# Performance work log

Measured on AMD Instinct MI355X. Metric: run time of the kernel, lower is better.

Reference implementation:

```python
import jax, jax.numpy as jnp
import numpy as np

D = 1024        # input_dim
H = 4096        # hidden_dim (expert FFN width)
RH = H // 2     # router hidden
E = 8           # expert_count
TOP_K = 2
N = 4096        # tokens
LN_EPS = 1e-5


def setup_inputs() -> dict:
    key = jax.random.key(0)
    ks = jax.random.split(key, 12)
    s_d = 1.0 / np.sqrt(D)
    s_h = 1.0 / np.sqrt(H)
    s_rh = 1.0 / np.sqrt(RH)
    return {
        "x": jax.random.normal(ks[0], (N, D), jnp.float32),
        "ln_g": jnp.ones((D,), jnp.float32),
        "ln_b": jnp.zeros((D,), jnp.float32),
        # router: Linear(D, RH) -> ReLU -> Linear(RH, E)
        "rw1": jax.random.uniform(ks[1], (D, RH), jnp.float32, -s_d, s_d),
        "rb1": jax.random.uniform(ks[2], (RH,), jnp.float32, -s_d, s_d),
        "rw2": jax.random.uniform(ks[3], (RH, E), jnp.float32, -s_rh, s_rh),
        "rb2": jax.random.uniform(ks[4], (E,), jnp.float32, -s_rh, s_rh),
        # experts: E x (Linear(D, H) -> ReLU -> Linear(H, D)); dropout is identity in eval
        "ew1": jax.random.uniform(ks[5], (E, D, H), jnp.float32, -s_d, s_d),
        "eb1": jax.random.uniform(ks[6], (E, H), jnp.float32, -s_d, s_d),
        "ew2": jax.random.uniform(ks[7], (E, H, D), jnp.float32, -s_h, s_h),
        "eb2": jax.random.uniform(ks[8], (E, D), jnp.float32, -s_h, s_h),
    }


def reference(x, ln_g, ln_b, rw1, rb1, rw2, rb2, ew1, eb1, ew2, eb2):
    residual = x
    # LayerNorm
    mu = jnp.mean(x, axis=-1, keepdims=True)
    var = jnp.mean(jnp.square(x - mu), axis=-1, keepdims=True)
    xn = (x - mu) * jax.lax.rsqrt(var + LN_EPS) * ln_g + ln_b
    # Router MLP + softmax + top-k with renormalized gates
    logits = jax.nn.relu(xn @ rw1 + rb1) @ rw2 + rb2          # [N, E]
    probs = jax.nn.softmax(logits, axis=-1)
    vals, idx = jax.lax.top_k(probs, TOP_K)                    # [N, K]
    vals = vals / jnp.sum(vals, axis=-1, keepdims=True)
    # combine weights per expert: [N, E]
    combine = jnp.sum(jax.nn.one_hot(idx, E, dtype=vals.dtype) * vals[..., None], axis=1)
    # dense grouped expert FFN: h [E, N, H], y [E, N, D]
    h = jax.nn.relu(jnp.einsum("nd,edh->enh", xn, ew1) + eb1[:, None, :])
    y = jnp.einsum("enh,ehd->end", h, ew2) + eb2[:, None, :]
    out = residual + jnp.einsum("end,ne->nd", y, combine)
    return out
```

## Files before the change

kernel.cpp:

```cpp
#include <hip/hip_runtime.h>
#include <stdint.h>

#define D_    1024
#define H_    4096
#define RH_   2048
#define E_    8
#define N_    4096
#define NK_   8192
#define MT256_MAX 39
#define DELTA_MARGIN 1e-4f
#define FIX_CAP 256

typedef __bf16 bf16x8 __attribute__((ext_vector_type(8)));
typedef float  f32x4  __attribute__((ext_vector_type(4)));


__device__ __forceinline__ unsigned short f2bf(float f) {
  union { float f; unsigned u; } v; v.f = f;
  unsigned r = v.u + 0x7fffu + ((v.u >> 16) & 1u);
  return (unsigned short)(r >> 16);
}
__device__ __forceinline__ float bf2f(unsigned short h) {
  union { unsigned u; float f; } v; v.u = ((unsigned)h) << 16;
  return v.f;
}

#define GLOAD16(gp, lp) \
  __builtin_amdgcn_global_load_lds((__attribute__((address_space(1))) void*)(void*)(gp), \
                                   (__attribute__((address_space(3))) void*)(lp), 16, 0, 0)

__global__ __launch_bounds__(256) void k_transpose(const float* __restrict__ in,
                                                   unsigned short* __restrict__ outH,
                                                   unsigned short* __restrict__ outL,
                                                   int R, int C) {
  __shared__ float t[32][33];
  const int b = blockIdx.z;
  const int c0 = blockIdx.x * 32, r0 = blockIdx.y * 32;
  const int lx = threadIdx.x & 31, ly = threadIdx.x >> 5;
  const long inB = (long)R * C;
  #pragma unroll
  for (int i = 0; i < 4; i++) {
    int r = r0 + ly + i * 8;
    t[ly + i * 8][lx] = in[b * inB + (long)r * C + c0 + lx];
  }
  __syncthreads();
  #pragma unroll
  for (int i = 0; i < 4; i++) {
    int c = c0 + ly + i * 8;
    float v = t[lx][ly + i * 8];
    unsigned short h = f2bf(v);
    long oi = b * inB + (long)c * R + r0 + lx;
    outH[oi] = h;
    if (outL) outL[oi] = f2bf(v - bf2f(h));
  }
}

__global__ __launch_bounds__(256) void k_layernorm(const float* __restrict__ x,
                                                   const float* __restrict__ g,
                                                   const float* __restrict__ b,
                                                   unsigned short* __restrict__ xnh,
                                                   unsigned short* __restrict__ xnl) {
  __shared__ float red[4];
  const int n = blockIdx.x, tid = threadIdx.x;
  float4 v = ((const float4*)(x + (long)n * D_))[tid];
  float s = v.x + v.y + v.z + v.w;
  #pragma unroll
  for (int o = 32; o >= 1; o >>= 1) s += __shfl_xor(s, o, 64);
  if ((tid & 63) == 0) red[tid >> 6] = s;
  __syncthreads();
  float mean = (red[0] + red[1] + red[2] + red[3]) * (1.f / D_);
  __syncthreads();
  float d0 = v.x - mean, d1 = v.y - mean, d2 = v.z - mean, d3 = v.w - mean;
  float ss = d0 * d0 + d1 * d1 + d2 * d2 + d3 * d3;
  #pragma unroll
  for (int o = 32; o >= 1; o >>= 1) ss += __shfl_xor(ss, o, 64);
  if ((tid & 63) == 0) red[tid >> 6] = ss;
  __syncthreads();
  float rstd = rsqrtf((red[0] + red[1] + red[2] + red[3]) * (1.f / D_) + 1e-5f);
  float4 gg = ((const float4*)g)[tid];
  float4 bb = ((const float4*)b)[tid];
  float xn0 = d0 * rstd * gg.x + bb.x;
  float xn1 = d1 * rstd * gg.y + bb.y;
  float xn2 = d2 * rstd * gg.z + bb.z;
  float xn3 = d3 * rstd * gg.w + bb.w;
  unsigned short h0 = f2bf(xn0), h1 = f2bf(xn1), h2 = f2bf(xn2), h3 = f2bf(xn3);
  ((ushort4*)xnh)[(long)n * 256 + tid] = make_ushort4(h0, h1, h2, h3);
  ((ushort4*)xnl)[(long)n * 256 + tid] = make_ushort4(
      f2bf(xn0 - bf2f(h0)), f2bf(xn1 - bf2f(h1)),
      f2bf(xn2 - bf2f(h2)), f2bf(xn3 - bf2f(h3)));
}

__global__ void k_init(int* ctl) { if (threadIdx.x < 46) ctl[threadIdx.x] = 0; }

__global__ __launch_bounds__(256) void k_router_gemm(const unsigned short* __restrict__ xh,
                                                     const unsigned short* __restrict__ xl,
                                                     const unsigned short* __restrict__ bhT,
                                                     const unsigned short* __restrict__ blT,
                                                     const float* __restrict__ rb1,
                                                     float* __restrict__ h_r) {
  __shared__ __align__(16) unsigned short Ah[128 * 32], Al[128 * 32], Bh[128 * 32], Bl[128 * 32];
  const int tid = threadIdx.x, lane = tid & 63, wid = tid >> 6;
  const int m0 = blockIdx.x * 128, n0 = blockIdx.y * 128;
  const int wm = wid >> 1, wn = wid & 1;
  const int seg0 = wid * 2;
  const int srow = lane >> 2;
  const int scol = (lane & 3) * 8;
  const long a0 = (long)(m0 + seg0 * 16 + srow) * D_ + scol;
  const long a1 = a0 + 16 * D_;
  const long b0 = (long)(n0 + seg0 * 16 + srow) * D_ + scol;
  const long b1 = b0 + 16 * D_;
  const int rl = lane & 15, kh8 = (lane >> 4) * 8;
  f32x4 acc[4][4];
  #pragma unroll
  for (int i = 0; i < 4; i++)
    #pragma unroll
    for (int j = 0; j < 4; j++) acc[i][j] = 0.f;

  for (int k0 = 0; k0 < D_; k0 += 32) {
    GLOAD16(xh + a0 + k0, Ah + seg0 * 512);
    GLOAD16(xh + a1 + k0, Ah + seg0 * 512 + 512);
    GLOAD16(xl + a0 + k0, Al + seg0 * 512);
    GLOAD16(xl + a1 + k0, Al + seg0 * 512 + 512);
    GLOAD16(bhT + b0 + k0, Bh + seg0 * 512);
    GLOAD16(bhT + b1 + k0, Bh + seg0 * 512 + 512);
    GLOAD16(blT + b0 + k0, Bl + seg0 * 512);
    GLOAD16(blT + b1 + k0, Bl + seg0 * 512 + 512);
    __syncthreads();
    bf16x8 bhf[4], blf[4];
    #pragma unroll
    for (int ni = 0; ni < 4; ni++) {
      int r = (wn * 64 + ni * 16 + rl) * 32 + kh8;
      bhf[ni] = *(const bf16x8*)(Bh + r);
      blf[ni] = *(const bf16x8*)(Bl + r);
    }
    #pragma unroll
    for (int mi = 0; mi < 4; mi++) {
      int r = (wm * 64 + mi * 16 + rl) * 32 + kh8;
      bf16x8 ah = *(const bf16x8*)(Ah + r);
      bf16x8 al = *(const bf16x8*)(Al + r);
      #pragma unroll
      for (int ni = 0; ni < 4; ni++) {
        acc[mi][ni] = __builtin_amdgcn_mfma_f32_16x16x32_bf16(ah, bhf[ni], acc[mi][ni], 0, 0, 0);
        acc[mi][ni] = __builtin_amdgcn_mfma_f32_16x16x32_bf16(ah, blf[ni], acc[mi][ni], 0, 0, 0);
        acc[mi][ni] = __builtin_amdgcn_mfma_f32_16x16x32_bf16(al, bhf[ni], acc[mi][ni], 0, 0, 0);
      }
    }
    __syncthreads();
  }
  const int rg4 = (lane >> 4) * 4;
  #pragma unroll
  for (int ni = 0; ni < 4; ni++) {
    int col = n0 + wn * 64 + ni * 16 + rl;
    float bias = rb1[col];
    #pragma unroll
    for (int mi = 0; mi < 4; mi++) {
      int row = m0 + wm * 64 + mi * 16 + rg4;
      #pragma unroll
      for (int r = 0; r < 4; r++) {
        float v = acc[mi][ni][r] + bias;
        h_r[(long)(row + r) * RH_ + col] = v > 0.f ? v : 0.f;
      }
    }
  }
}

__global__ __launch_bounds__(256) void k_logits_top2(const float* __restrict__ h_r,
                                                     const float* __restrict__ rw2,
                                                     const float* __restrict__ rb2,
                                                     int* __restrict__ sel, float* __restrict__ gate,
                                                     int* __restrict__ marked, int* __restrict__ mcount) {
  const int lane = threadIdx.x & 63, wid = threadIdx.x >> 6;
  const int n = blockIdx.x * 4 + wid;
  float p[8] = {0, 0, 0, 0, 0, 0, 0, 0};
  const float* hr = h_r + (long)n * RH_;
  for (int i = 0; i < RH_ / 64; i++) {
    int c = i * 64 + lane;
    float v = hr[c];
    float4 wa = ((const float4*)(rw2 + c * 8))[0];
    float4 wb = ((const float4*)(rw2 + c * 8))[1];
    p[0] += v * wa.x; p[1] += v * wa.y; p[2] += v * wa.z; p[3] += v * wa.w;
    p[4] += v * wb.x; p[5] += v * wb.y; p[6] += v * wb.z; p[7] += v * wb.w;
  }
  #pragma unroll
  for (int e = 0; e < 8; e++)
    #pragma unroll
    for (int s = 32; s >= 1; s >>= 1) p[e] += __shfl_xor(p[e], s, 64);
  if (lane == 0) {
    float l1 = -1e30f, l2 = -1e30f, l3 = -1e30f; int e1 = 0, e2 = 0;
    #pragma unroll
    for (int e = 0; e < 8; e++) {
      float v = p[e] + rb2[e];
      if (v > l1)      { l3 = l2; l2 = l1; e2 = e1; l1 = v; e1 = e; }
      else if (v > l2) { l3 = l2; l2 = v; e2 = e; }
      else if (v > l3) { l3 = v; }
    }
    float g1 = 1.f / (1.f + expf(l2 - l1));
    sel[n * 2] = e1; sel[n * 2 + 1] = e2;
    gate[n * 2] = g1; gate[n * 2 + 1] = 1.f - g1;
    if (l2 - l3 < DELTA_MARGIN) { int i = atomicAdd(mcount, 1); marked[i] = n; }
  }
}

__global__ __launch_bounds__(256) void k_fixup1(const float* __restrict__ x,
                                                const float* __restrict__ ln_g, const float* __restrict__ ln_b,
                                                const float* __restrict__ rw1, const float* __restrict__ rb1,
                                                const int* __restrict__ marked, const int* __restrict__ mcount,
                                                double* __restrict__ hsbuf) {
  __shared__ float xs[D_];
  __shared__ float redf[4];
  __shared__ double part[64][5];
  const int tid = threadIdx.x;
  int cnt = *mcount; if (cnt > FIX_CAP) cnt = FIX_CAP;
  const int blkTok = blockIdx.x >> 5;
  const int chunk  = blockIdx.x & 31;
  for (int mi = blkTok; mi < cnt; mi += FIX_CAP) {
    const int n = marked[mi];
    float4 v = ((const float4*)(x + (long)n * D_))[tid];
    float s = v.x + v.y + v.z + v.w;
    #pragma unroll
    for (int o = 32; o >= 1; o >>= 1) s += __shfl_xor(s, o, 64);
    if ((tid & 63) == 0) redf[tid >> 6] = s;
    __syncthreads();
    float mean = (redf[0] + redf[1] + redf[2] + redf[3]) * (1.f / D_);
    __syncthreads();
    float d0 = v.x - mean, d1 = v.y - mean, d2 = v.z - mean, d3 = v.w - mean;
    float ss = d0 * d0 + d1 * d1 + d2 * d2 + d3 * d3;
    #pragma unroll
    for (int o = 32; o >= 1; o >>= 1) ss += __shfl_xor(ss, o, 64);
    if ((tid & 63) == 0) redf[tid >> 6] = ss;
    __syncthreads();
    float rstd = rsqrtf((redf[0] + redf[1] + redf[2] + redf[3]) * (1.f / D_) + 1e-5f);
    float4 gg = ((const float4*)ln_g)[tid];
    float4 bb = ((const float4*)ln_b)[tid];
    xs[tid * 4 + 0] = d0 * rstd * gg.x + bb.x;
    xs[tid * 4 + 1] = d1 * rstd * gg.y + bb.y;
    xs[tid * 4 + 2] = d2 * rstd * gg.z + bb.z;
    xs[tid * 4 + 3] = d3 * rstd * gg.w + bb.w;
    __syncthreads();
    const int lcol = tid & 63, prt = tid >> 6;
    const int col = chunk * 64 + lcol;
    const float* rp = rw1 + (long)(prt * 256) * RH_ + col;
    const float* xp = xs + prt * 256;
    double a0 = 0, a1 = 0, a2 = 0, a3 = 0;
    #pragma unroll 4
    for (int d = 0; d < 256; d += 4) {
      float w0 = rp[(long)(d + 0) * RH_];
      float w1 = rp[(long)(d + 1) * RH_];
      float w2 = rp[(long)(d + 2) * RH_];
      float w3 = rp[(long)(d + 3) * RH_];
      a0 += (double)xp[d + 0] * (double)w0;
      a1 += (double)xp[d + 1] * (double)w1;
      a2 += (double)xp[d + 2] * (double)w2;
      a3 += (double)xp[d + 3] * (double)w3;
    }
    part[lcol][prt] = (a0 + a1) + (a2 + a3);
    __syncthreads();
    if (tid < 64) {
      double a = (part[tid][0] + part[tid][1]) + (part[tid][2] + part[tid][3])
               + (double)rb1[chunk * 64 + tid];
      hsbuf[(long)mi * RH_ + chunk * 64 + tid] = a > 0.0 ? a : 0.0;
    }
    __syncthreads();
  }
}

__global__ __launch_bounds__(256) void k_fixup2(const double* __restrict__ hsbuf,
                                                const float* __restrict__ rw2, const float* __restrict__ rb2,
                                                const int* __restrict__ marked, const int* __restrict__ mcount,
                                                int* __restrict__ sel, float* __restrict__ gate) {
  __shared__ double red2[256];
  const int tid = threadIdx.x;
  int cnt = *mcount; if (cnt > FIX_CAP) cnt = FIX_CAP;
  for (int mi = blockIdx.x; mi < cnt; mi += gridDim.x) {
    const int n = marked[mi];
    const double* hs = hsbuf + (long)mi * RH_;
    const int e = tid & 7, ch = tid >> 3;
    double pp = 0.0;
    for (int c = ch * 64; c < ch * 64 + 64; c++) pp += hs[c] * (double)rw2[c * 8 + e];
    red2[tid] = pp;
    __syncthreads();
    if (tid < 128) red2[tid] += red2[tid + 128];
    __syncthreads();
    if (tid < 64) red2[tid] += red2[tid + 64];
    __syncthreads();
    if (tid < 32) red2[tid] += red2[tid + 32];
    __syncthreads();
    if (tid < 16) red2[tid] += red2[tid + 16];
    __syncthreads();
    if (tid < 8) red2[tid] += red2[tid + 8];
    __syncthreads();
    if (tid == 0) {
      double l1 = -1e300, l2 = -1e300; int e1 = 0, e2 = 0;
      for (int ee = 0; ee < 8; ee++) {
        double vv = red2[ee] + (double)rb2[ee];
        if (vv > l1)      { l2 = l1; e2 = e1; l1 = vv; e1 = ee; }
        else if (vv > l2) { l2 = vv; e2 = ee; }
      }
      double g1 = 1.0 / (1.0 + exp(l2 - l1));
      sel[n * 2] = e1; sel[n * 2 + 1] = e2;
      gate[n * 2] = (float)g1; gate[n * 2 + 1] = (float)(1.0 - g1);
    }
    __syncthreads();
  }
}

__global__ void k_count(const int* __restrict__ sel, int* ctl) {
  int n = blockIdx.x * 256 + threadIdx.x;
  if (n >= N_) return;
  atomicAdd(&ctl[sel[n * 2]], 1);
  atomicAdd(&ctl[sel[n * 2 + 1]], 1);
}
__global__ void k_offsets(int* ctl) {
  if (threadIdx.x == 0 && blockIdx.x == 0) {
    int t = 0, t2 = 0;
    for (int e = 0; e < 8; e++) {
      ctl[8 + e] = t; ctl[26 + e] = t; ctl[36 + e] = t2;
      t += ctl[e]; t2 += (ctl[e] + 255) >> 8;
    }
    ctl[16] = t; ctl[44] = t2;
  }
}
__global__ void k_scatter(const int* __restrict__ sel, int* ctl,
                          int* __restrict__ perm, int* __restrict__ pos) {
  int n = blockIdx.x * 256 + threadIdx.x;
  if (n >= N_) return;
  #pragma unroll
  for (int k = 0; k < 2; k++) {
    int e = sel[n * 2 + k];
    int p = atomicAdd(&ctl[26 + e], 1);
    perm[p] = n;
    pos[n * 2 + k] = p;
  }
}

template <int KD, int BN, bool GATHER, bool RELU_BF16, bool MTFAST>
__global__ __launch_bounds__(512, 2) void k_gemm_expert2(const unsigned short* __restrict__ A,
                                                         const unsigned short* __restrict__ BT,
                                                         const float* __restrict__ bias,
                                                         const int* __restrict__ ctl,
                                                         const int* __restrict__ perm,
                                                         unsigned short* __restrict__ outBF,
                                                         float* __restrict__ outF32, int NB) {
  const int* cnt = ctl; const int* off = ctl + 8; const int* toff = ctl + 36;
  const int NX = gridDim.x, MT = gridDim.y;
  const int nwg = NX * MT;
  const int F = blockIdx.y * NX + blockIdx.x;
  const int q = nwg >> 3, r8 = nwg & 7;
  const int xcd = F & 7, j = F >> 3;
  const int L = (xcd < r8 ? xcd * (q + 1) : r8 * (q + 1) + (xcd - r8) * q) + j;
  int mt, nt;
  if (MTFAST) { mt = L % MT; nt = L / MT; }
  else        { nt = L % NX; mt = L / NX; }
  if (mt >= toff[8]) return;
  int e = 0;
  #pragma unroll
  for (int i = 0; i < 7; i++) if (toff[i + 1] <= mt) e = i + 1;
  const int ltile = mt - toff[e];
  const int g0 = off[e] + ltile * 256;
  int vrows = cnt[e] - ltile * 256; if (vrows > 256) vrows = 256;
  const int n0 = nt * BN;

  __shared__ __align__(16) unsigned short At[256 * 32], Bt[BN * 32];
  __shared__ int pidx[256];
  const int tid = threadIdx.x, lane = tid & 63, wid = tid >> 6;
  if constexpr (GATHER) {
    if (tid < 256) {
      int g = g0 + tid, gmax = off[e] + cnt[e] - 1;
      pidx[tid] = perm[g <= gmax ? g : gmax];
    }
    __syncthreads();
  }
  const int srow = lane >> 2;
  const int scol = (lane & 3) * 8;
  const int arow0 = wid * 32 + srow;
  const int arow1 = arow0 + 16;
  long aa0, aa1;
  if constexpr (GATHER) {
    aa0 = (long)pidx[arow0] * KD + scol;
    aa1 = (long)pidx[arow1] * KD + scol;
  } else {
    aa0 = (long)(g0 + arow0) * KD + scol;
    aa1 = aa0 + (long)16 * KD;
  }
  const long bbase = (long)e * NB * KD;
  long ba0, ba1;
  if constexpr (BN == 256) {
    ba0 = bbase + (long)(n0 + wid * 32 + srow) * KD + scol;
    ba1 = ba0 + (long)16 * KD;
  } else {
    ba0 = bbase + (long)(n0 + wid * 16 + srow) * KD + scol;
    ba1 = 0;
  }

  constexpr int WN = BN / 64;
  constexpr int MR = (BN == 256) ? 8 : 4;
  constexpr int WROW = (BN == 256) ? 128 : 64;
  const int wm = wid / WN, wn = wid % WN;
  const int rl = lane & 15, kh8 = (lane >> 4) * 8;
  f32x4 acc[MR][4];
  #pragma unroll
  for (int i = 0; i < MR; i++)
    #pragma unroll
    for (int jj = 0; jj < 4; jj++) acc[i][jj] = 0.f;

  for (int k0 = 0; k0 < KD; k0 += 32) {
    GLOAD16(A + aa0 + k0, At + (wid * 2) * 512);
    GLOAD16(A + aa1 + k0, At + (wid * 2) * 512 + 512);
    if constexpr (BN == 256) {
      GLOAD16(BT + ba0 + k0, Bt + (wid * 2) * 512);
      GLOAD16(BT + ba1 + k0, Bt + (wid * 2) * 512 + 512);
    } else {
      GLOAD16(BT + ba0 + k0, Bt + wid * 512);
    }
    __syncthreads();
    bf16x8 bfr[4];
    #pragma unroll
    for (int ni = 0; ni < 4; ni++)
      bfr[ni] = *(const bf16x8*)(Bt + (wn * 64 + ni * 16 + rl) * 32 + kh8);
    #pragma unroll
    for (int mi = 0; mi < MR; mi++) {
      bf16x8 af = *(const bf16x8*)(At + (wm * WROW + mi * 16 + rl) * 32 + kh8);
      #pragma unroll
      for (int ni = 0; ni < 4; ni++)
        acc[mi][ni] = __builtin_amdgcn_mfma_f32_16x16x32_bf16(af, bfr[ni], acc[mi][ni], 0, 0, 0);
    }
    __syncthreads();
  }
  const int rg4 = (lane >> 4) * 4;
  #pragma unroll
  for (int ni = 0; ni < 4; ni++) {
    int col = n0 + wn * 64 + ni * 16 + rl;
    float bv = bias[(long)e * NB + col];
    #pragma unroll
    for (int mi = 0; mi < MR; mi++) {
      int lrow = wm * WROW + mi * 16 + rg4;
      #pragma unroll
      for (int r = 0; r < 4; r++) {
        if (lrow + r < vrows) {
          float v = acc[mi][ni][r] + bv;
          long idx = (long)(g0 + lrow + r) * NB + col;
          if constexpr (RELU_BF16) outBF[idx] = f2bf(v > 0.f ? v : 0.f);
          else outF32[idx] = v;
        }
      }
    }
  }
}

__global__ __launch_bounds__(256) void k_combine(const float* __restrict__ x,
                                                 const float* __restrict__ y_buf,
                                                 const int* __restrict__ pos,
                                                 const float* __restrict__ gate,
                                                 float* __restrict__ out) {
  const int n = blockIdx.x, t = threadIdx.x;
  const float g0 = gate[n * 2], g1 = gate[n * 2 + 1];
  const long p0 = pos[n * 2], p1 = pos[n * 2 + 1];
  float4 xv = ((const float4*)(x + (long)n * D_))[t];
  float4 a = ((const float4*)(y_buf + p0 * D_))[t];
  float4 b = ((const float4*)(y_buf + p1 * D_))[t];
  float4 o;
  o.x = xv.x + g0 * a.x + g1 * b.x;
  o.y = xv.y + g0 * a.y + g1 * b.y;
  o.z = xv.z + g0 * a.z + g1 * b.z;
  o.w = xv.w + g0 * a.w + g1 * b.w;
  ((float4*)(out + (long)n * D_))[t] = o;
}

extern "C" void kernel_launch(void* const* d_in, const int* in_sizes, int n_in,
                              void* d_out, int out_size, void* d_ws, size_t ws_size,
                              hipStream_t stream) {
  const float* x    = (const float*)d_in[0];
  const float* ln_g = (const float*)d_in[1];
  const float* ln_b = (const float*)d_in[2];
  const float* rw1  = (const float*)d_in[3];
  const float* rb1  = (const float*)d_in[4];
  const float* rw2  = (const float*)d_in[5];
  const float* rb2  = (const float*)d_in[6];
  const float* ew1  = (const float*)d_in[7];
  const float* eb1  = (const float*)d_in[8];
  const float* ew2  = (const float*)d_in[9];
  const float* eb2  = (const float*)d_in[10];
  float* out = (float*)d_out;

  char* w = (char*)d_ws;
  size_t off = 0;
  auto alloc = [&](size_t bytes) -> char* {
    char* p = w + off;
    off += (bytes + 255) & ~(size_t)255;
    return p;
  };
  unsigned short* ew1T  = (unsigned short*)alloc((size_t)E_ * H_ * D_ * 2);
  unsigned short* ew2T  = (unsigned short*)alloc((size_t)E_ * D_ * H_ * 2);
  unsigned short* rw1hT = (unsigned short*)alloc((size_t)RH_ * D_ * 2);
  unsigned short* rw1lT = (unsigned short*)alloc((size_t)RH_ * D_ * 2);
  unsigned short* xnh   = (unsigned short*)alloc((size_t)N_ * D_ * 2);
  unsigned short* xnl   = (unsigned short*)alloc((size_t)N_ * D_ * 2);
  float*          h_r   = (float*)alloc((size_t)N_ * RH_ * 4);
  unsigned short* h_buf = (unsigned short*)alloc((size_t)(NK_ + 256) * H_ * 2);
  float*          y_buf = (float*)alloc((size_t)(NK_ + 256) * D_ * 4);
  double*         hsbuf = (double*)alloc((size_t)FIX_CAP * RH_ * 8);
  int*   sel    = (int*)alloc((size_t)N_ * 2 * 4);
  float* gate   = (float*)alloc((size_t)N_ * 2 * 4);
  int*   marked = (int*)alloc((size_t)N_ * 4);
  int*   perm   = (int*)alloc((size_t)NK_ * 4);
  int*   pos    = (int*)alloc((size_t)N_ * 2 * 4);
  int*   ctl    = (int*)alloc(64 * 4);

  k_transpose<<<dim3(H_ / 32, D_ / 32, E_), 256, 0, stream>>>(ew1, ew1T, nullptr, D_, H_);
  k_transpose<<<dim3(D_ / 32, H_ / 32, E_), 256, 0, stream>>>(ew2, ew2T, nullptr, H_, D_);
  k_transpose<<<dim3(RH_ / 32, D_ / 32, 1), 256, 0, stream>>>(rw1, rw1hT, rw1lT, D_, RH_);
  k_layernorm<<<N_, 256, 0, stream>>>(x, ln_g, ln_b, xnh, xnl);
  k_init<<<1, 64, 0, stream>>>(ctl);
  k_router_gemm<<<dim3(N_ / 128, RH_ / 128), 256, 0, stream>>>(xnh, xnl, rw1hT, rw1lT, rb1, h_r);
  k_logits_top2<<<N_ / 4, 256, 0, stream>>>(h_r, rw2, rb2, sel, gate, marked, ctl + 34);
  k_fixup1<<<FIX_CAP * 32, 256, 0, stream>>>(x, ln_g, ln_b, rw1, rb1, marked, ctl + 34, hsbuf);
  k_fixup2<<<64, 256, 0, stream>>>(hsbuf, rw2, rb2, marked, ctl + 34, sel, gate);
  k_count<<<N_ / 256, 256, 0, stream>>>(sel, ctl);
  k_offsets<<<1, 1, 0, stream>>>(ctl);
  k_scatter<<<N_ / 256, 256, 0, stream>>>(sel, ctl, perm, pos);
  k_gemm_expert2<D_, 256, true, true, true><<<dim3(H_ / 256, MT256_MAX), 512, 0, stream>>>(
      xnh, ew1T, eb1, ctl, perm, h_buf, nullptr, H_);
  k_gemm_expert2<H_, 128, false, false, false><<<dim3(D_ / 128, MT256_MAX), 512, 0, stream>>>(
      h_buf, ew2T, eb2, ctl, perm, nullptr, y_buf, D_);
  k_combine<<<N_, 256, 0, stream>>>(x, y_buf, pos, gate, out);

  (void)in_sizes; (void)n_in; (void)out_size; (void)ws_size;
}
```

Before: 599.7 us.

## Double-buffer expert GEMM LDS tiles with K=64 steps to overlap loads and MFMA

Rewrites the expert grouped GEMM main loop to use two LDS buffers with a K-step of 64, so the next tile's global-to-LDS loads are issued while the MFMAs run on the current one. This halves the number of barriers per K and drops the separate gather-index LDS staging, reading perm directly into per-thread addresses. LDS use rises to roughly 128KB per block for the first GEMM, and the launch bound no longer asks for two blocks per CU, which may lower occupancy.

```diff
diff --git a/kernel.cpp b/kernel.cpp
--- a/kernel.cpp
+++ b/kernel.cpp
@@ -334,13 +334,13 @@
 }
 
 template <int KD, int BN, bool GATHER, bool RELU_BF16, bool MTFAST>
-__global__ __launch_bounds__(512, 2) void k_gemm_expert2(const unsigned short* __restrict__ A,
-                                                         const unsigned short* __restrict__ BT,
-                                                         const float* __restrict__ bias,
-                                                         const int* __restrict__ ctl,
-                                                         const int* __restrict__ perm,
-                                                         unsigned short* __restrict__ outBF,
-                                                         float* __restrict__ outF32, int NB) {
+__global__ __launch_bounds__(512) void k_gemm_expert3(const unsigned short* __restrict__ A,
+                                                      const unsigned short* __restrict__ BT,
+                                                      const float* __restrict__ bias,
+                                                      const int* __restrict__ ctl,
+                                                      const int* __restrict__ perm,
+                                                      unsigned short* __restrict__ outBF,
+                                                      float* __restrict__ outF32, int NB) {
   const int* cnt = ctl; const int* off = ctl + 8; const int* toff = ctl + 36;
   const int NX = gridDim.x, MT = gridDim.y;
   const int nwg = NX * MT;
@@ -360,72 +360,83 @@
   int vrows = cnt[e] - ltile * 256; if (vrows > 256) vrows = 256;
   const int n0 = nt * BN;
 
-  __shared__ __align__(16) unsigned short At[256 * 32], Bt[BN * 32];
-  __shared__ int pidx[256];
+  __shared__ __align__(16) unsigned short At[2][256 * 64];
+  __shared__ __align__(16) unsigned short Bt[2][BN * 64];
   const int tid = threadIdx.x, lane = tid & 63, wid = tid >> 6;
-  if constexpr (GATHER) {
-    if (tid < 256) {
-      int g = g0 + tid, gmax = off[e] + cnt[e] - 1;
-      pidx[tid] = perm[g <= gmax ? g : gmax];
-    }
-    __syncthreads();
-  }
-  const int srow = lane >> 2;
-  const int scol = (lane & 3) * 8;
-  const int arow0 = wid * 32 + srow;
-  const int arow1 = arow0 + 16;
-  long aa0, aa1;
-  if constexpr (GATHER) {
-    aa0 = (long)pidx[arow0] * KD + scol;
-    aa1 = (long)pidx[arow1] * KD + scol;
-  } else {
-    aa0 = (long)(g0 + arow0) * KD + scol;
-    aa1 = aa0 + (long)16 * KD;
-  }
+  const int lr8 = lane >> 3;
+  const int lk8 = (lane & 7) * 8;
+  long aa[4];
+  #pragma unroll
+  for (int i = 0; i < 4; i++) {
+    int row = wid * 32 + i * 8 + lr8;
+    long arow;
+    if constexpr (GATHER) {
+      int g = g0 + row, gmax = off[e] + cnt[e] - 1;
+      arow = perm[g <= gmax ? g : gmax];
+    } else {
+      arow = g0 + row;
+    }
+    aa[i] = arow * (long)KD + lk8;
+  }
+  constexpr int BI = BN / 64;
   const long bbase = (long)e * NB * KD;
-  long ba0, ba1;
-  if constexpr (BN == 256) {
-    ba0 = bbase + (long)(n0 + wid * 32 + srow) * KD + scol;
-    ba1 = ba0 + (long)16 * KD;
-  } else {
-    ba0 = bbase + (long)(n0 + wid * 16 + srow) * KD + scol;
-    ba1 = 0;
+  long bb[BI];
+  #pragma unroll
+  for (int i = 0; i < BI; i++) {
+    int row = n0 + wid * (BN / 8) + i * 8 + lr8;
+    bb[i] = bbase + (long)row * KD + lk8;
   }
 
   constexpr int WN = BN / 64;
-  constexpr int MR = (BN == 256) ? 8 : 4;
-  constexpr int WROW = (BN == 256) ? 128 : 64;
+  constexpr int MR = 256 / (8 / WN) / 16;
+  constexpr int WROW = MR * 16;
   const int wm = wid / WN, wn = wid % WN;
   const int rl = lane & 15, kh8 = (lane >> 4) * 8;
+
   f32x4 acc[MR][4];
   #pragma unroll
   for (int i = 0; i < MR; i++)
     #pragma unroll
     for (int jj = 0; jj < 4; jj++) acc[i][jj] = 0.f;
 
-  for (int k0 = 0; k0 < KD; k0 += 32) {
-    GLOAD16(A + aa0 + k0, At + (wid * 2) * 512);
-    GLOAD16(A + aa1 + k0, At + (wid * 2) * 512 + 512);
-    if constexpr (BN == 256) {
-      GLOAD16(BT + ba0 + k0, Bt + (wid * 2) * 512);
-      GLOAD16(BT + ba1 + k0, Bt + (wid * 2) * 512 + 512);
-    } else {
-      GLOAD16(BT + ba0 + k0, Bt + wid * 512);
-    }
-    __syncthreads();
-    bf16x8 bfr[4];
-    #pragma unroll
-    for (int ni = 0; ni < 4; ni++)
-      bfr[ni] = *(const bf16x8*)(Bt + (wn * 64 + ni * 16 + rl) * 32 + kh8);
-    #pragma unroll
-    for (int mi = 0; mi < MR; mi++) {
-      bf16x8 af = *(const bf16x8*)(At + (wm * WROW + mi * 16 + rl) * 32 + kh8);
+  constexpr int NT = KD / 64;
+
+  auto stage = [&](int bi, int k0) {
+    #pragma unroll
+    for (int i = 0; i < 4; i++)
+      GLOAD16(A + aa[i] + k0, &At[bi][(wid * 32 + i * 8) * 64]);
+    #pragma unroll
+    for (int i = 0; i < BI; i++)
+      GLOAD16(BT + bb[i] + k0, &Bt[bi][(wid * (BN / 8) + i * 8) * 64]);
+  };
+  auto compute = [&](int bi) {
+    #pragma unroll
+    for (int kk = 0; kk < 2; kk++) {
+      bf16x8 bfr[4];
       #pragma unroll
       for (int ni = 0; ni < 4; ni++)
-        acc[mi][ni] = __builtin_amdgcn_mfma_f32_16x16x32_bf16(af, bfr[ni], acc[mi][ni], 0, 0, 0);
-    }
-    __syncthreads();
-  }
+        bfr[ni] = *(const bf16x8*)(&Bt[bi][(wn * 64 + ni * 16 + rl) * 64 + kk * 32 + kh8]);
+      #pragma unroll
+      for (int mi = 0; mi < MR; mi++) {
+        bf16x8 af = *(const bf16x8*)(&At[bi][(wm * WROW + mi * 16 + rl) * 64 + kk * 32 + kh8]);
+        #pragma unroll
+        for (int ni = 0; ni < 4; ni++)
+          acc[mi][ni] = __builtin_amdgcn_mfma_f32_16x16x32_bf16(af, bfr[ni], acc[mi][ni], 0, 0, 0);
+      }
+    }
+  };
+
+  stage(0, 0);
+  __syncthreads();
+  int cur = 0;
+  for (int t = 0; t < NT - 1; ++t) {
+    stage(cur ^ 1, (t + 1) * 64);
+    compute(cur);
+    __syncthreads();
+    cur ^= 1;
+  }
+  compute(cur);
+
   const int rg4 = (lane >> 4) * 4;
   #pragma unroll
   for (int ni = 0; ni < 4; ni++) {
@@ -518,9 +529,9 @@
   k_count<<<N_ / 256, 256, 0, stream>>>(sel, ctl);
   k_offsets<<<1, 1, 0, stream>>>(ctl);
   k_scatter<<<N_ / 256, 256, 0, stream>>>(sel, ctl, perm, pos);
-  k_gemm_expert2<D_, 256, true, true, true><<<dim3(H_ / 256, MT256_MAX), 512, 0, stream>>>(
+  k_gemm_expert3<D_, 256, true, true, true><<<dim3(H_ / 256, MT256_MAX), 512, 0, stream>>>(
       xnh, ew1T, eb1, ctl, perm, h_buf, nullptr, H_);
-  k_gemm_expert2<H_, 128, false, false, false><<<dim3(D_ / 128, MT256_MAX), 512, 0, stream>>>(
+  k_gemm_expert3<H_, 128, false, false, false><<<dim3(D_ / 128, MT256_MAX), 512, 0, stream>>>(
       h_buf, ew2T, eb2, ctl, perm, nullptr, y_buf, D_);
   k_combine<<<N_, 256, 0, stream>>>(x, y_buf, pos, gate, out);
 
```

After: 729.5 us. 21.6% more time.
